# Optimization experiments

Hardware: AMD Instinct MI355X
Metric: run time of the kernel (lower is better)

## Reference

```python
import jax, jax.numpy as jnp
import numpy as np

N_NODES = 50000
N_EDGES = 600000
D = 128


def _mean_agg(h, src, dst, n_nodes):
    # DGL SAGEConv 'mean': mean of incoming src features per dst node; 0 for isolated nodes
    s = jax.ops.segment_sum(h[src], dst, num_segments=n_nodes)  # [N, d]
    deg = jax.ops.segment_sum(jnp.ones_like(dst, dtype=h.dtype), dst, num_segments=n_nodes)
    return s / jnp.maximum(deg, 1.0)[:, None]


def setup_inputs() -> dict:
    key = jax.random.key(0)
    ks = jax.random.split(key, 10)
    sc = 1.0 / np.sqrt(D)
    return {
        "x": jax.random.normal(ks[0], (N_NODES, D), jnp.float32),
        "e": jax.random.normal(ks[1], (N_EDGES, D), jnp.float32),
        "src": jax.random.randint(ks[2], (N_EDGES,), 0, N_NODES, jnp.int32),
        "dst": jax.random.randint(ks[3], (N_EDGES,), 0, N_NODES, jnp.int32),
        "W1_self": jax.random.normal(ks[4], (D, D), jnp.float32) * sc,
        "W1_neigh": jax.random.normal(ks[5], (D, D), jnp.float32) * sc,
        "b1": jnp.zeros((D,), jnp.float32),
        "W2_self": jax.random.normal(ks[6], (D, D), jnp.float32) * sc,
        "W2_neigh": jax.random.normal(ks[7], (D, D), jnp.float32) * sc,
        "b2": jnp.zeros((D,), jnp.float32),
        "Wp": jax.random.normal(ks[8], (2 * D, 3), jnp.float32) * (1.0 / np.sqrt(2 * D)),
        "bp": jnp.zeros((3,), jnp.float32),
    }


def reference(x, e, src, dst, W1_self, W1_neigh, b1, W2_self, W2_neigh, b2, Wp, bp):
    n = x.shape[0]
    # SAGEConv 1 (mean) + ReLU
    agg1 = _mean_agg(x, src, dst, n)
    h = jax.nn.relu(x @ W1_self + agg1 @ W1_neigh + b1)
    # SAGEConv 2 (mean)
    agg2 = _mean_agg(h, src, dst, n)
    h = h @ W2_self + agg2 @ W2_neigh + b2
    # MLPPredictor: per-edge gather, concat, linear (edge feature e unused in score)
    he = jnp.concatenate([h[src], h[dst]], axis=1)  # [E, 2D]
    score = he @ Wp + bp  # [E, 3]
    return score
```

## Files before the change

kernel.cpp:

```cpp
#include <hip/hip_runtime.h>
#include <hip/hip_bf16.h>


typedef __attribute__((ext_vector_type(8))) short bf16x8;
typedef __attribute__((ext_vector_type(4))) float f32x4;

static __device__ __forceinline__ float bf16lo(unsigned u) {
    return __uint_as_float(u << 16);
}
static __device__ __forceinline__ float bf16hi(unsigned u) {
    return __uint_as_float(u & 0xffff0000u);
}
static __device__ __forceinline__ unsigned short f2bf(float f) {
    unsigned u = __float_as_uint(f);
    unsigned r = 0x7fffu + ((u >> 16) & 1u);
    return (unsigned short)((u + r) >> 16);
}
static __device__ __forceinline__ unsigned pack_bf162(float a, float b) {
    return (unsigned)f2bf(a) | ((unsigned)f2bf(b) << 16);
}

#define SORT_BLOCKS 128

__global__ __launch_bounds__(256) void k_misc(
    const float* __restrict__ x, unsigned short* __restrict__ xb,
    const int* __restrict__ dst, int* __restrict__ H,
    const float* __restrict__ W1s, const float* __restrict__ W1n,
    unsigned short* __restrict__ Wt1,
    const float* __restrict__ W2s, const float* __restrict__ W2n,
    const float* __restrict__ Wp, const float* __restrict__ b2,
    const float* __restrict__ bp, float* __restrict__ Wc,
    float* __restrict__ bconst, int N, int E, int CHUNK)
{
    const int nCvt = (N * 32 + 255) / 256;
    const int b = blockIdx.x;
    const int t = threadIdx.x;

    if (b < nCvt) {
        int i = b * 256 + t;
        if (i < N * 32) {
            float4 v = ((const float4*)x)[i];
            uint2 o;
            o.x = pack_bf162(v.x, v.y);
            o.y = pack_bf162(v.z, v.w);
            *(uint2*)(xb + (size_t)i * 4) = o;
        }
    } else if (b < nCvt + SORT_BLOCKS) {
        __shared__ int hist[256];
        hist[t] = 0;
        __syncthreads();
        int blk = b - nCvt;
        int start = blk * CHUNK;
        int end = min(start + CHUNK, E);
        for (int e = start + t; e < end; e += 256)
            atomicAdd(&hist[((unsigned)dst[e]) >> 8], 1);
        __syncthreads();
        H[blk * 256 + t] = hist[t];
    } else if (b < nCvt + SORT_BLOCKS + 128) {
        int id = (b - nCvt - SORT_BLOCKS) * 256 + t;
        int k = id >> 7, n = id & 127;
        float v = (k < 128) ? W1s[k * 128 + n] : W1n[(k - 128) * 128 + n];
        Wt1[n * 256 + k] = f2bf(v);
    } else {
        for (int id = t; id < 1539; id += 256) {
            if (id < 1536) {
                int c = id / 12, j = id % 12;
                int q = j / 3, jj = j % 3;
                const float* W2 = (q == 0 || q == 2) ? W2s : W2n;
                int wpoff = (q < 2) ? 0 : 128;
                float s = 0.f;
                for (int m = 0; m < 128; ++m)
                    s += W2[c * 128 + m] * Wp[(wpoff + m) * 3 + jj];
                Wc[c * 12 + j] = s;
            } else {
                int jj = id - 1536;
                float s = bp[jj];
                for (int m = 0; m < 128; ++m)
                    s += b2[m] * (Wp[m * 3 + jj] + Wp[(128 + m) * 3 + jj]);
                bconst[jj] = s;
            }
        }
    }
}

__global__ __launch_bounds__(256) void k_s2(int* __restrict__ H,
                                            int* __restrict__ bucketBase,
                                            int NB, int E) {
    const int t = threadIdx.x;
    int tot = 0;
    for (int blk = 0; blk < SORT_BLOCKS; ++blk) tot += H[blk * 256 + t];
    __shared__ int lt[256];
    lt[t] = tot;
    __syncthreads();
    for (int off = 1; off < 256; off <<= 1) {
        int u = (t >= off) ? lt[t - off] : 0;
        __syncthreads();
        lt[t] += u;
        __syncthreads();
    }
    int excl = lt[t] - tot;
    if (t < NB) bucketBase[t] = excl;
    if (t == 0) bucketBase[NB] = E;
    int run = excl;
    for (int blk = 0; blk < SORT_BLOCKS; ++blk) {
        int h = H[blk * 256 + t];
        H[blk * 256 + t] = run;
        run += h;
    }
}

__global__ __launch_bounds__(256) void k_s3(const int* __restrict__ src,
                                            const int* __restrict__ dst,
                                            const int* __restrict__ H,
                                            int* __restrict__ packed,
                                            int E, int CHUNK) {
    __shared__ int cur[256];
    const int t = threadIdx.x, blk = blockIdx.x;
    cur[t] = H[blk * 256 + t];
    __syncthreads();
    int start = blk * CHUNK, end = min(start + CHUNK, E);
    for (int e = start + t; e < end; e += 256) {
        int d = dst[e];
        int p = atomicAdd(&cur[((unsigned)d) >> 8], 1);
        packed[p] = (src[e] & 0xFFFF) | ((d & 255) << 16);
    }
}

__global__ __launch_bounds__(256) void k_s4(const int* __restrict__ packed,
                                            const int* __restrict__ bucketBase,
                                            int* __restrict__ eidx,
                                            int* __restrict__ cursor,
                                            float* __restrict__ fdeg,
                                            float* __restrict__ invdeg, int N) {
    const int t = threadIdx.x, b = blockIdx.x;
    const int rb = bucketBase[b], re = bucketBase[b + 1];
    __shared__ int cnt[256];
    __shared__ int lt[256];
    __shared__ int cur[256];
    cnt[t] = 0;
    __syncthreads();
    for (int i = rb + t; i < re; i += 256)
        atomicAdd(&cnt[(packed[i] >> 16) & 255], 1);
    __syncthreads();
    int v = cnt[t];
    lt[t] = v;
    __syncthreads();
    for (int off = 1; off < 256; off <<= 1) {
        int u = (t >= off) ? lt[t - off] : 0;
        __syncthreads();
        lt[t] += u;
        __syncthreads();
    }
    int excl = lt[t] - v;
    int node = b * 256 + t;
    if (node < N) {
        cursor[node] = rb + excl + v;
        fdeg[node] = (float)v;
        invdeg[node] = 1.0f / fmaxf((float)v, 1.0f);
    }
    cur[t] = rb + excl;
    __syncthreads();
    for (int i = rb + t; i < re; i += 256) {
        int p = packed[i];
        int pos = atomicAdd(&cur[(p >> 16) & 255], 1);
        eidx[pos] = p & 0xFFFF;
    }
}

__global__ __launch_bounds__(256) void k_gemm_fused(
    const unsigned short* __restrict__ xb,
    const int* __restrict__ eidx, const int* __restrict__ cursor,
    const float* __restrict__ fdeg, const float* __restrict__ invdeg,
    const unsigned short* __restrict__ Wt, const float* __restrict__ bias,
    const float* __restrict__ Wc, float* __restrict__ P, int N)
{
    __shared__ __align__(16) char sW[65536];
    __shared__ float sWc[1536];
    const int t = threadIdx.x;
    const int wave = t >> 6, lane = t & 63;
    const int nodeBase = blockIdx.x * 128 + wave * 32;
    const int lrow = lane & 15, lk = lane >> 4;
    const int r0 = nodeBase + lrow, r1 = nodeBase + 16 + lrow;

    int* eidxL = (int*)sW;
    const int nb0 = blockIdx.x * 128;
    const int lastN = min(nb0 + 127, N - 1);
    const int estart = cursor[nb0] - (int)fdeg[nb0];
    const int eend = cursor[lastN];
    const int ecnt = eend - estart;
    const bool ldsOK = (ecnt <= 16384);
    if (ldsOK) {
        for (int i = t; i < ecnt; i += 256) eidxL[i] = eidx[estart + i];
    }
    __syncthreads();

    union { bf16x8 v; unsigned u[4]; } afrag0[4], afrag1[4];

#define GATHER_NODE(R, EP, OFF, AF)                                          \
    {                                                                        \
        float agg[4][8];                                                     \
        _Pragma("unroll") for (int ksb = 0; ksb < 4; ++ksb)                  \
            _Pragma("unroll") for (int i = 0; i < 8; ++i) agg[ksb][i] = 0.f; \
        if ((R) < N) {                                                       \
            int d = (int)fdeg[R];                                            \
            int o = (OFF);                                                   \
            int j = 0;                                                       \
            for (; j + 2 <= d; j += 2) {                                     \
                int s0 = (EP)[o + j], s1 = (EP)[o + j + 1];                  \
                const unsigned short* row0 = xb + (size_t)s0 * 128 + lk * 8; \
                const unsigned short* row1 = xb + (size_t)s1 * 128 + lk * 8; \
                uint4 v0[4], v1[4];                                          \
                _Pragma("unroll") for (int ksb = 0; ksb < 4; ++ksb) {        \
                    v0[ksb] = *(const uint4*)(row0 + ksb * 32);              \
                    v1[ksb] = *(const uint4*)(row1 + ksb * 32);              \
                }                                                            \
                _Pragma("unroll") for (int ksb = 0; ksb < 4; ++ksb) {        \
                    agg[ksb][0] += bf16lo(v0[ksb].x);                        \
                    agg[ksb][1] += bf16hi(v0[ksb].x);                        \
                    agg[ksb][2] += bf16lo(v0[ksb].y);                        \
                    agg[ksb][3] += bf16hi(v0[ksb].y);                        \
                    agg[ksb][4] += bf16lo(v0[ksb].z);                        \
                    agg[ksb][5] += bf16hi(v0[ksb].z);                        \
                    agg[ksb][6] += bf16lo(v0[ksb].w);                        \
                    agg[ksb][7] += bf16hi(v0[ksb].w);                        \
                    agg[ksb][0] += bf16lo(v1[ksb].x);                        \
                    agg[ksb][1] += bf16hi(v1[ksb].x);                        \
                    agg[ksb][2] += bf16lo(v1[ksb].y);                        \
                    agg[ksb][3] += bf16hi(v1[ksb].y);                        \
                    agg[ksb][4] += bf16lo(v1[ksb].z);                        \
                    agg[ksb][5] += bf16hi(v1[ksb].z);                        \
                    agg[ksb][6] += bf16lo(v1[ksb].w);                        \
                    agg[ksb][7] += bf16hi(v1[ksb].w);                        \
                }                                                            \
            }                                                                \
            if (j < d) {                                                     \
                int s0 = (EP)[o + j];                                        \
                const unsigned short* row0 = xb + (size_t)s0 * 128 + lk * 8; \
                _Pragma("unroll") for (int ksb = 0; ksb < 4; ++ksb) {        \
                    uint4 v0 = *(const uint4*)(row0 + ksb * 32);             \
                    agg[ksb][0] += bf16lo(v0.x);                             \
                    agg[ksb][1] += bf16hi(v0.x);                             \
                    agg[ksb][2] += bf16lo(v0.y);                             \
                    agg[ksb][3] += bf16hi(v0.y);                             \
                    agg[ksb][4] += bf16lo(v0.z);                             \
                    agg[ksb][5] += bf16hi(v0.z);                             \
                    agg[ksb][6] += bf16lo(v0.w);                             \
                    agg[ksb][7] += bf16hi(v0.w);                             \
                }                                                            \
            }                                                                \
            float sc = invdeg[R];                                            \
            _Pragma("unroll") for (int ksb = 0; ksb < 4; ++ksb)              \
                _Pragma("unroll") for (int i = 0; i < 4; ++i)                \
                    AF[ksb].u[i] = pack_bf162(agg[ksb][2 * i] * sc,          \
                                              agg[ksb][2 * i + 1] * sc);     \
        } else {                                                             \
            _Pragma("unroll") for (int ksb = 0; ksb < 4; ++ksb)              \
                _Pragma("unroll") for (int i = 0; i < 4; ++i)                \
                    AF[ksb].u[i] = 0u;                                       \
        }                                                                    \
    }

    if (ldsOK) {
        GATHER_NODE(r0, eidxL, (r0 < N ? cursor[r0] - (int)fdeg[r0] - estart : 0), afrag0)
        GATHER_NODE(r1, eidxL, (r1 < N ? cursor[r1] - (int)fdeg[r1] - estart : 0), afrag1)
    } else {
        GATHER_NODE(r0, eidx, (r0 < N ? cursor[r0] - (int)fdeg[r0] : 0), afrag0)
        GATHER_NODE(r1, eidx, (r1 < N ? cursor[r1] - (int)fdeg[r1] : 0), afrag1)
    }
#undef GATHER_NODE

    __syncthreads();
#pragma unroll
    for (int i = 0; i < 16; ++i) {
        int o = (i * 256 + t) * 16;
        int n = o >> 9;
        int c = o & 511;
        int sw = (n << 9) | (c ^ ((n & 7) << 4));
        *(float4*)&sW[sw] = *(const float4*)((const char*)Wt + o);
    }
    for (int i = t; i < 1536; i += 256) sWc[i] = Wc[i];

    f32x4 acc[2][8];
#pragma unroll
    for (int rs = 0; rs < 2; ++rs)
#pragma unroll
        for (int nb = 0; nb < 8; ++nb) acc[rs][nb] = (f32x4){0.f, 0.f, 0.f, 0.f};

    __syncthreads();

    for (int ks = 0; ks < 8; ++ks) {
        bf16x8 a0, a1;
        if (ks < 4) {
            const int kk = ks * 32 + lk * 8;
            a0 = (bf16x8){};
            a1 = (bf16x8){};
            if (r0 < N) a0 = *(const bf16x8*)(xb + (size_t)r0 * 128 + kk);
            if (r1 < N) a1 = *(const bf16x8*)(xb + (size_t)r1 * 128 + kk);
        } else {
            a0 = afrag0[ks - 4].v;
            a1 = afrag1[ks - 4].v;
        }
        const int cbase = ks * 64 + lk * 16;
#pragma unroll
        for (int nb = 0; nb < 8; ++nb) {
            int n = nb * 16 + lrow;
            int sw = (n << 9) | (cbase ^ ((n & 7) << 4));
            bf16x8 b = *(const bf16x8*)&sW[sw];
            acc[0][nb] = __builtin_amdgcn_mfma_f32_16x16x32_bf16(a0, b, acc[0][nb], 0, 0, 0);
            acc[1][nb] = __builtin_amdgcn_mfma_f32_16x16x32_bf16(a1, b, acc[1][nb], 0, 0, 0);
        }
    }

#pragma unroll
    for (int rs = 0; rs < 2; ++rs) {
        float hval[8][4];
#pragma unroll
        for (int nb = 0; nb < 8; ++nb) {
            float bv = bias[nb * 16 + lrow];
#pragma unroll
            for (int r = 0; r < 4; ++r)
                hval[nb][r] = fmaxf(acc[rs][nb][r] + bv, 0.f);
        }
#pragma unroll
        for (int r = 0; r < 4; ++r) {
            float pj[12];
#pragma unroll
            for (int j = 0; j < 12; ++j) pj[j] = 0.f;
#pragma unroll
            for (int nb = 0; nb < 8; ++nb) {
                float hv = hval[nb][r];
                const float* wrow = &sWc[(nb * 16 + lrow) * 12];
#pragma unroll
                for (int j = 0; j < 12; ++j) pj[j] += hv * wrow[j];
            }
#pragma unroll
            for (int off = 8; off; off >>= 1) {
#pragma unroll
                for (int j = 0; j < 12; ++j) pj[j] += __shfl_xor(pj[j], off, 64);
            }
            int node = nodeBase + rs * 16 + lk * 4 + r;
            if (lrow == 0 && node < N) {
                float* prow = &P[(size_t)node * 16];
                *(float4*)(prow + 0)  = make_float4(pj[0], pj[1], pj[2], pj[6]);
                *(float4*)(prow + 4)  = make_float4(pj[7], pj[8], 0.f, 0.f);
                *(float4*)(prow + 8)  = make_float4(pj[3], pj[4], pj[5], pj[9]);
                *(float4*)(prow + 12) = make_float4(pj[10], pj[11], 0.f, 0.f);
            }
        }
    }
}

__global__ __launch_bounds__(256) void k_agg3(const float* __restrict__ P,
                                              const int* __restrict__ eidx,
                                              const int* __restrict__ cursor,
                                              const float* __restrict__ fdeg,
                                              const float* __restrict__ invdeg,
                                              float* __restrict__ ps4,
                                              float* __restrict__ pd4, int N) {
    int g = (blockIdx.x * blockDim.x + threadIdx.x) >> 3;
    int j = threadIdx.x & 7;
    if (g >= N || j >= 6) return;
    int d = (int)fdeg[g];
    int o = cursor[g] - d;
    float a = 0.f;
    int i = 0;
    for (; i + 2 <= d; i += 2) {
        int s0 = eidx[o + i], s1 = eidx[o + i + 1];
        a += P[(size_t)s0 * 16 + 8 + j];
        a += P[(size_t)s1 * 16 + 8 + j];
    }
    if (i < d) a += P[(size_t)eidx[o + i] * 16 + 8 + j];
    a *= invdeg[g];
    float r = P[(size_t)g * 16 + j] + a;
    if (j < 3)
        ps4[(size_t)g * 4 + j] = r;
    else
        pd4[(size_t)g * 4 + (j - 3)] = r;
}

__global__ void k_edge(const float4* __restrict__ ps4, const float4* __restrict__ pd4,
                       const int* __restrict__ src, const int* __restrict__ dst,
                       const float* __restrict__ bconst, float* __restrict__ out, int E)
{
    int e = blockIdx.x * blockDim.x + threadIdx.x;
    if (e >= E) return;
    float4 a = ps4[src[e]];
    float4 b = pd4[dst[e]];
    out[(size_t)e * 3 + 0] = a.x + b.x + bconst[0];
    out[(size_t)e * 3 + 1] = a.y + b.y + bconst[1];
    out[(size_t)e * 3 + 2] = a.z + b.z + bconst[2];
}

extern "C" void kernel_launch(void* const* d_in, const int* in_sizes, int n_in,
                              void* d_out, int out_size, void* d_ws, size_t ws_size,
                              hipStream_t stream)
{
    const float* x   = (const float*)d_in[0];
    const int*   src = (const int*)d_in[2];
    const int*   dst = (const int*)d_in[3];
    const float* W1s = (const float*)d_in[4];
    const float* W1n = (const float*)d_in[5];
    const float* b1  = (const float*)d_in[6];
    const float* W2s = (const float*)d_in[7];
    const float* W2n = (const float*)d_in[8];
    const float* b2  = (const float*)d_in[9];
    const float* Wp  = (const float*)d_in[10];
    const float* bp  = (const float*)d_in[11];
    const int N = in_sizes[0] / 128;
    const int E = in_sizes[2];
    float* out = (float*)d_out;

    const int NB = (N + 255) / 256;
    const int CHUNK = (E + SORT_BLOCKS - 1) / SORT_BLOCKS;

    char* wsp = (char*)d_ws;
    auto alloc = [&](size_t bytes) { char* p = wsp; wsp += (bytes + 255) & ~(size_t)255; return p; };
    float* fdeg     = (float*)alloc((size_t)N * 4);
    float* invdeg   = (float*)alloc((size_t)N * 4);
    int*   cursor   = (int*)alloc((size_t)N * 4);
    int*   eidx     = (int*)alloc((size_t)E * 4);
    int*   packed   = (int*)alloc((size_t)E * 4);
    int*   H        = (int*)alloc((size_t)SORT_BLOCKS * 256 * 4);
    int*   bucketBase = (int*)alloc(260 * 4);
    unsigned short* xb  = (unsigned short*)alloc((size_t)N * 128 * 2);
    unsigned short* Wt1 = (unsigned short*)alloc(256 * 128 * 2);
    float* Wc     = (float*)alloc(1536 * 4);
    float* bconst = (float*)alloc(256);
    float* P      = (float*)alloc((size_t)N * 16 * 4);
    float* ps4    = (float*)alloc((size_t)N * 16);
    float* pd4    = (float*)alloc((size_t)N * 16);

    const int nCvt = (N * 32 + 255) / 256;
    k_misc<<<nCvt + SORT_BLOCKS + 129, 256, 0, stream>>>(
        x, xb, dst, H, W1s, W1n, Wt1, W2s, W2n, Wp, b2, bp, Wc, bconst, N, E, CHUNK);

    k_s2<<<1, 256, 0, stream>>>(H, bucketBase, NB, E);
    k_s3<<<SORT_BLOCKS, 256, 0, stream>>>(src, dst, H, packed, E, CHUNK);
    k_s4<<<NB, 256, 0, stream>>>(packed, bucketBase, eidx, cursor, fdeg, invdeg, N);

    k_gemm_fused<<<(N + 127) / 128, 256, 0, stream>>>(xb, eidx, cursor, fdeg, invdeg,
                                                      Wt1, b1, Wc, P, N);

    k_agg3<<<(N * 8 + 255) / 256, 256, 0, stream>>>(P, eidx, cursor, fdeg, invdeg,
                                                    ps4, pd4, N);

    k_edge<<<(E + 255) / 256, 256, 0, stream>>>((const float4*)ps4, (const float4*)pd4,
                                                src, dst, bconst, out, E);
}
```

Baseline: 161.4 us.

## Fuse bucket scan into scatter, halve GEMM LDS, vectorize agg3

Removes the single-block scan kernel: every scatter block now recomputes the column totals, the bucket prefix and its own per-block offset, and block 0 writes bucketBase. The fused GEMM now stages the weight tile in two 32KB halves instead of one 64KB buffer, and launch bounds request 3 blocks per SM for higher occupancy. The price is an extra barrier round and a smaller LDS threshold for caching edge indices. The agg3 kernel now uses one thread per node with float4 loads instead of 8 lanes per node.

```diff
diff --git a/kernel.cpp b/kernel.cpp
--- a/kernel.cpp
+++ b/kernel.cpp
@@ -83,40 +83,35 @@
     }
 }
 
-__global__ __launch_bounds__(256) void k_s2(int* __restrict__ H,
-                                            int* __restrict__ bucketBase,
-                                            int NB, int E) {
-    const int t = threadIdx.x;
-    int tot = 0;
-    for (int blk = 0; blk < SORT_BLOCKS; ++blk) tot += H[blk * 256 + t];
-    __shared__ int lt[256];
-    lt[t] = tot;
-    __syncthreads();
-    for (int off = 1; off < 256; off <<= 1) {
-        int u = (t >= off) ? lt[t - off] : 0;
-        __syncthreads();
-        lt[t] += u;
-        __syncthreads();
-    }
-    int excl = lt[t] - tot;
-    if (t < NB) bucketBase[t] = excl;
-    if (t == 0) bucketBase[NB] = E;
-    int run = excl;
-    for (int blk = 0; blk < SORT_BLOCKS; ++blk) {
-        int h = H[blk * 256 + t];
-        H[blk * 256 + t] = run;
-        run += h;
-    }
-}
-
 __global__ __launch_bounds__(256) void k_s3(const int* __restrict__ src,
                                             const int* __restrict__ dst,
                                             const int* __restrict__ H,
                                             int* __restrict__ packed,
+                                            int* __restrict__ bucketBase,
                                             int E, int CHUNK) {
+    __shared__ int lt[256];
     __shared__ int cur[256];
     const int t = threadIdx.x, blk = blockIdx.x;
-    cur[t] = H[blk * 256 + t];
+    int tot = 0, pre = 0;
+    for (int b = 0; b < SORT_BLOCKS; ++b) {
+        int h = H[b * 256 + t];
+        pre += (b < blk) ? h : 0;
+        tot += h;
+    }
+    lt[t] = tot;
+    __syncthreads();
+    for (int off = 1; off < 256; off <<= 1) {
+        int u = (t >= off) ? lt[t - off] : 0;
+        __syncthreads();
+        lt[t] += u;
+        __syncthreads();
+    }
+    int excl = lt[t] - tot;
+    cur[t] = excl + pre;
+    if (blk == 0) {
+        bucketBase[t] = excl;
+        if (t == 0) bucketBase[256] = E;
+    }
     __syncthreads();
     int start = blk * CHUNK, end = min(start + CHUNK, E);
     for (int e = start + t; e < end; e += 256) {
@@ -167,14 +162,14 @@
     }
 }
 
-__global__ __launch_bounds__(256) void k_gemm_fused(
+__global__ __launch_bounds__(256, 3) void k_gemm_fused(
     const unsigned short* __restrict__ xb,
     const int* __restrict__ eidx, const int* __restrict__ cursor,
     const float* __restrict__ fdeg, const float* __restrict__ invdeg,
     const unsigned short* __restrict__ Wt, const float* __restrict__ bias,
     const float* __restrict__ Wc, float* __restrict__ P, int N)
 {
-    __shared__ __align__(16) char sW[65536];
+    __shared__ __align__(16) char sW[32768];
     __shared__ float sWc[1536];
     const int t = threadIdx.x;
     const int wave = t >> 6, lane = t & 63;
@@ -188,7 +183,7 @@
     const int estart = cursor[nb0] - (int)fdeg[nb0];
     const int eend = cursor[lastN];
     const int ecnt = eend - estart;
-    const bool ldsOK = (ecnt <= 16384);
+    const bool ldsOK = (ecnt <= 8192);
     if (ldsOK) {
         for (int i = t; i < ecnt; i += 256) eidxL[i] = eidx[estart + i];
     }
@@ -269,45 +264,49 @@
     }
 #undef GATHER_NODE
 
-    __syncthreads();
-#pragma unroll
-    for (int i = 0; i < 16; ++i) {
-        int o = (i * 256 + t) * 16;
-        int n = o >> 9;
-        int c = o & 511;
-        int sw = (n << 9) | (c ^ ((n & 7) << 4));
-        *(float4*)&sW[sw] = *(const float4*)((const char*)Wt + o);
-    }
-    for (int i = t; i < 1536; i += 256) sWc[i] = Wc[i];
-
     f32x4 acc[2][8];
 #pragma unroll
     for (int rs = 0; rs < 2; ++rs)
 #pragma unroll
         for (int nb = 0; nb < 8; ++nb) acc[rs][nb] = (f32x4){0.f, 0.f, 0.f, 0.f};
 
-    __syncthreads();
-
-    for (int ks = 0; ks < 8; ++ks) {
-        bf16x8 a0, a1;
-        if (ks < 4) {
-            const int kk = ks * 32 + lk * 8;
-            a0 = (bf16x8){};
-            a1 = (bf16x8){};
-            if (r0 < N) a0 = *(const bf16x8*)(xb + (size_t)r0 * 128 + kk);
-            if (r1 < N) a1 = *(const bf16x8*)(xb + (size_t)r1 * 128 + kk);
-        } else {
-            a0 = afrag0[ks - 4].v;
-            a1 = afrag1[ks - 4].v;
-        }
-        const int cbase = ks * 64 + lk * 16;
-#pragma unroll
-        for (int nb = 0; nb < 8; ++nb) {
-            int n = nb * 16 + lrow;
-            int sw = (n << 9) | (cbase ^ ((n & 7) << 4));
-            bf16x8 b = *(const bf16x8*)&sW[sw];
-            acc[0][nb] = __builtin_amdgcn_mfma_f32_16x16x32_bf16(a0, b, acc[0][nb], 0, 0, 0);
-            acc[1][nb] = __builtin_amdgcn_mfma_f32_16x16x32_bf16(a1, b, acc[1][nb], 0, 0, 0);
+    for (int half = 0; half < 2; ++half) {
+        __syncthreads();
+#pragma unroll
+        for (int i = 0; i < 8; ++i) {
+            int idx = i * 256 + t;
+            int n = idx >> 4;
+            int c = (idx & 15) << 4;
+            int sw = (n << 8) | (c ^ ((n & 7) << 4));
+            *(uint4*)&sW[sw] =
+                *(const uint4*)((const char*)Wt + n * 512 + half * 256 + c);
+        }
+        if (half == 0)
+            for (int i = t; i < 1536; i += 256) sWc[i] = Wc[i];
+        __syncthreads();
+
+        for (int ks2 = 0; ks2 < 4; ++ks2) {
+            const int ks = half * 4 + ks2;
+            bf16x8 a0, a1;
+            if (half == 0) {
+                const int kk = ks * 32 + lk * 8;
+                a0 = (bf16x8){};
+                a1 = (bf16x8){};
+                if (r0 < N) a0 = *(const bf16x8*)(xb + (size_t)r0 * 128 + kk);
+                if (r1 < N) a1 = *(const bf16x8*)(xb + (size_t)r1 * 128 + kk);
+            } else {
+                a0 = afrag0[ks2].v;
+                a1 = afrag1[ks2].v;
+            }
+            const int cbase = ks2 * 64 + lk * 16;
+#pragma unroll
+            for (int nb = 0; nb < 8; ++nb) {
+                int n = nb * 16 + lrow;
+                int sw = (n << 8) | (cbase ^ ((n & 7) << 4));
+                bf16x8 b = *(const bf16x8*)&sW[sw];
+                acc[0][nb] = __builtin_amdgcn_mfma_f32_16x16x32_bf16(a0, b, acc[0][nb], 0, 0, 0);
+                acc[1][nb] = __builtin_amdgcn_mfma_f32_16x16x32_bf16(a1, b, acc[1][nb], 0, 0, 0);
+            }
         }
     }
 
@@ -355,27 +354,34 @@
                                               const int* __restrict__ cursor,
                                               const float* __restrict__ fdeg,
                                               const float* __restrict__ invdeg,
-                                              float* __restrict__ ps4,
-                                              float* __restrict__ pd4, int N) {
-    int g = (blockIdx.x * blockDim.x + threadIdx.x) >> 3;
-    int j = threadIdx.x & 7;
-    if (g >= N || j >= 6) return;
+                                              float4* __restrict__ ps4,
+                                              float4* __restrict__ pd4, int N) {
+    int g = blockIdx.x * 256 + threadIdx.x;
+    if (g >= N) return;
     int d = (int)fdeg[g];
     int o = cursor[g] - d;
-    float a = 0.f;
+    float a0 = 0.f, a1 = 0.f, a2 = 0.f, a3 = 0.f, a4 = 0.f, a5 = 0.f;
     int i = 0;
     for (; i + 2 <= d; i += 2) {
         int s0 = eidx[o + i], s1 = eidx[o + i + 1];
-        a += P[(size_t)s0 * 16 + 8 + j];
-        a += P[(size_t)s1 * 16 + 8 + j];
-    }
-    if (i < d) a += P[(size_t)eidx[o + i] * 16 + 8 + j];
-    a *= invdeg[g];
-    float r = P[(size_t)g * 16 + j] + a;
-    if (j < 3)
-        ps4[(size_t)g * 4 + j] = r;
-    else
-        pd4[(size_t)g * 4 + (j - 3)] = r;
+        float4 u0 = *(const float4*)&P[(size_t)s0 * 16 + 8];
+        float4 u1 = *(const float4*)&P[(size_t)s0 * 16 + 12];
+        float4 w0 = *(const float4*)&P[(size_t)s1 * 16 + 8];
+        float4 w1 = *(const float4*)&P[(size_t)s1 * 16 + 12];
+        a0 += u0.x; a1 += u0.y; a2 += u0.z; a3 += u0.w; a4 += u1.x; a5 += u1.y;
+        a0 += w0.x; a1 += w0.y; a2 += w0.z; a3 += w0.w; a4 += w1.x; a5 += w1.y;
+    }
+    if (i < d) {
+        int s0 = eidx[o + i];
+        float4 u0 = *(const float4*)&P[(size_t)s0 * 16 + 8];
+        float4 u1 = *(const float4*)&P[(size_t)s0 * 16 + 12];
+        a0 += u0.x; a1 += u0.y; a2 += u0.z; a3 += u0.w; a4 += u1.x; a5 += u1.y;
+    }
+    float sc = invdeg[g];
+    float4 s0v = *(const float4*)&P[(size_t)g * 16];
+    float4 s1v = *(const float4*)&P[(size_t)g * 16 + 4];
+    ps4[g] = make_float4(s0v.x + a0 * sc, s0v.y + a1 * sc, s0v.z + a2 * sc, 0.f);
+    pd4[g] = make_float4(s0v.w + a3 * sc, s1v.x + a4 * sc, s1v.y + a5 * sc, 0.f);
 }
 
 __global__ void k_edge(const float4* __restrict__ ps4, const float4* __restrict__ pd4,
@@ -434,15 +440,14 @@
     k_misc<<<nCvt + SORT_BLOCKS + 129, 256, 0, stream>>>(
         x, xb, dst, H, W1s, W1n, Wt1, W2s, W2n, Wp, b2, bp, Wc, bconst, N, E, CHUNK);
 
-    k_s2<<<1, 256, 0, stream>>>(H, bucketBase, NB, E);
-    k_s3<<<SORT_BLOCKS, 256, 0, stream>>>(src, dst, H, packed, E, CHUNK);
+    k_s3<<<SORT_BLOCKS, 256, 0, stream>>>(src, dst, H, packed, bucketBase, E, CHUNK);
     k_s4<<<NB, 256, 0, stream>>>(packed, bucketBase, eidx, cursor, fdeg, invdeg, N);
 
     k_gemm_fused<<<(N + 127) / 128, 256, 0, stream>>>(xb, eidx, cursor, fdeg, invdeg,
                                                       Wt1, b1, Wc, P, N);
 
-    k_agg3<<<(N * 8 + 255) / 256, 256, 0, stream>>>(P, eidx, cursor, fdeg, invdeg,
-                                                    ps4, pd4, N);
+    k_agg3<<<(N + 255) / 256, 256, 0, stream>>>(P, eidx, cursor, fdeg, invdeg,
+                                                (float4*)ps4, (float4*)pd4, N);
 
     k_edge<<<(E + 255) / 256, 256, 0, stream>>>((const float4*)ps4, (const float4*)pd4,
                                                 src, dst, bconst, out, E);
```

Result: no change. 163.2 us (+1.1%).
